# Optimization experiments

Measured on AMD Instinct MI355X. Metric: run time of the kernel, lower is better.

## Reference

```python
import jax, jax.numpy as jnp
import numpy as np

N_NODES = 50000


def gcn_conv(x, W, b, src, dst):
    # PyG GCNConv: lin (no bias) -> add self-loops -> symmetric deg norm ->
    # scatter-add messages to target nodes -> add bias.
    n = x.shape[0]
    xw = x @ W  # [N, H]
    loops = jnp.arange(n, dtype=src.dtype)
    s = jnp.concatenate([src, loops])
    d = jnp.concatenate([dst, loops])
    deg = jax.ops.segment_sum(jnp.ones(d.shape[0], dtype=x.dtype), d, num_segments=n)
    dinv = deg ** -0.5  # deg >= 1 due to self-loops
    norm = dinv[s] * dinv[d]  # [E+N]
    msg = xw[s] * norm[:, None]  # gather + scale, [E+N, H]
    out = jax.ops.segment_sum(msg, d, num_segments=n)  # scatter-add
    return out + b


def setup_inputs() -> dict:
    key = jax.random.key(0)
    ks = jax.random.split(key, 8)
    in_feats, hidden, out_feats, p = 64, 64, 32, 4
    x = jax.random.normal(ks[0], (N_NODES, in_feats), dtype=jnp.float32)
    edge_index = jax.random.randint(ks[1], (2, 800000), 0, N_NODES, dtype=jnp.int64)
    s1 = (1.0 / in_feats) ** 0.5
    s2 = (1.0 / hidden) ** 0.5
    W1 = jax.random.uniform(ks[2], (in_feats, hidden), jnp.float32, -s1, s1)
    b1 = jnp.zeros((hidden,), jnp.float32)
    W2 = jax.random.uniform(ks[3], (hidden, hidden), jnp.float32, -s2, s2)
    b2 = jnp.zeros((hidden,), jnp.float32)
    Wr = jax.random.uniform(ks[4], (hidden, out_feats * p), jnp.float32, -s2, s2)
    br = jax.random.uniform(ks[5], (out_feats * p,), jnp.float32, -s2, s2)
    return {"x": x, "edge_index": edge_index, "W1": W1, "b1": b1,
            "W2": W2, "b2": b2, "Wr": Wr, "br": br}


def reference(x, edge_index, W1, b1, W2, b2, Wr, br):
    src, dst = edge_index[0], edge_index[1]
    h = jax.nn.relu(gcn_conv(x, W1, b1, src, dst))
    h = jax.nn.relu(gcn_conv(h, W2, b2, src, dst))
    g = jnp.mean(h, axis=0, keepdims=True)  # [1, hidden]
    out = (g @ Wr + br).reshape(32, 4)  # (out_feats, p)
    return out
```

## Files before the change

### kernel.cpp

```cpp
#include <hip/hip_runtime.h>
#include <math.h>


#define CH 4096
#define MAXNB 1024

__global__ __launch_bounds__(256) void k_bucket_hist(const int* __restrict__ dst,
                                                     int* __restrict__ histmat,
                                                     int E, int NB) {
    __shared__ int ih[MAXNB];
    int t = threadIdx.x;
    for (int k = t; k < NB; k += 256) ih[k] = 0;
    __syncthreads();
    int base = blockIdx.x * CH;
    for (int i = 0; i < CH; i += 256) {
        int e = base + i + t;
        if (e < E) atomicAdd(&ih[dst[e] >> 6], 1);
    }
    __syncthreads();
    for (int k = t; k < NB; k += 256) histmat[(size_t)blockIdx.x * NB + k] = ih[k];
}

__global__ __launch_bounds__(256) void k_colscan(int* __restrict__ histmat,
                                                 int* __restrict__ tot,
                                                 int NB, int nch) {
    int k = blockIdx.x * 256 + threadIdx.x;
    if (k >= NB) return;
    int run = 0;
    int b = 0;
    for (; b + 8 <= nch; b += 8) {
        int v[8];
#pragma unroll
        for (int u = 0; u < 8; u++) v[u] = histmat[(size_t)(b + u) * NB + k];
#pragma unroll
        for (int u = 0; u < 8; u++) {
            int x = v[u];
            histmat[(size_t)(b + u) * NB + k] = run;
            run += x;
        }
    }
    for (; b < nch; b++) {
        int x = histmat[(size_t)b * NB + k];
        histmat[(size_t)b * NB + k] = run;
        run += x;
    }
    tot[k] = run;
}

__global__ __launch_bounds__(256) void k_scanb(const int* __restrict__ tot,
                                               int* __restrict__ bstart,
                                               int* __restrict__ offsets,
                                               int NB, int E, int n) {
    __shared__ int sc[256];
    __shared__ int carry;
    int t = threadIdx.x;
    if (t == 0) carry = 0;
    __syncthreads();
    int nchunk = (NB + 255) / 256;
    for (int c = 0; c < nchunk; c++) {
        int idx = c * 256 + t;
        int v = (idx < NB) ? tot[idx] : 0;
        sc[t] = v;
        __syncthreads();
        for (int off = 1; off < 256; off <<= 1) {
            int x = (t >= off) ? sc[t - off] : 0;
            __syncthreads();
            sc[t] += x;
            __syncthreads();
        }
        if (idx < NB) bstart[idx] = sc[t] - v + carry;
        __syncthreads();
        if (t == 0) carry += sc[255];
        __syncthreads();
    }
    if (t == 0) { bstart[NB] = E; offsets[n] = E; }
}

__global__ __launch_bounds__(256) void k_bucket_scatter(const int* __restrict__ src,
                                                        const int* __restrict__ dst,
                                                        const int* __restrict__ histmat,
                                                        const int* __restrict__ bstart,
                                                        int* __restrict__ staged,
                                                        int E, int NB) {
    __shared__ int cur[MAXNB];
    int t = threadIdx.x;
    for (int k = t; k < NB; k += 256)
        cur[k] = bstart[k] + histmat[(size_t)blockIdx.x * NB + k];
    __syncthreads();
    int base = blockIdx.x * CH;
    for (int i = 0; i < CH; i += 256) {
        int e = base + i + t;
        if (e < E) {
            int d = dst[e];
            int pos = atomicAdd(&cur[d >> 6], 1);
            staged[pos] = (src[e] << 6) | (d & 63);
        }
    }
}

__global__ __launch_bounds__(256) void k_local_sort(const int* __restrict__ staged,
                                                    const int* __restrict__ bstart,
                                                    int* __restrict__ csr_src,
                                                    int* __restrict__ offsets,
                                                    float* __restrict__ dinv, int n) {
    __shared__ int cnt[64];
    __shared__ int pos[64];
    __shared__ int cur[64];
    int t = threadIdx.x;
    if (t < 64) cnt[t] = 0;
    __syncthreads();
    int k = blockIdx.x;
    int beg = bstart[k], end = bstart[k + 1];
    for (int e = beg + t; e < end; e += 256) atomicAdd(&cnt[staged[e] & 63], 1);
    __syncthreads();
    if (t == 0) {
        int run = 0;
        for (int i = 0; i < 64; i++) { pos[i] = run; run += cnt[i]; }
    }
    __syncthreads();
    if (t < 64) {
        cur[t] = pos[t];
        int node = k * 64 + t;
        if (node < n) {
            offsets[node] = beg + pos[t];
            dinv[node] = 1.0f / sqrtf((float)(cnt[t] + 1));
        }
    }
    __syncthreads();
    for (int e = beg + t; e < end; e += 256) {
        int pk = staged[e];
        int p = atomicAdd(&cur[pk & 63], 1);
        csr_src[beg + p] = pk >> 6;
    }
}

__global__ __launch_bounds__(256) void k_gemm_scale(const float* __restrict__ X,
                                                    const float* __restrict__ W,
                                                    const float* __restrict__ dinv,
                                                    float* __restrict__ Y, int n) {
    __shared__ float Ws[64 * 64];
    __shared__ float xs[16][64];
    int t = threadIdx.x, w = t >> 6, f = t & 63;
    const float4* W4 = (const float4*)W;
    float4* Ws4 = (float4*)Ws;
#pragma unroll
    for (int j = 0; j < 4; j++) Ws4[t + 256 * j] = W4[t + 256 * j];
    int r0 = blockIdx.x * 16;
#pragma unroll
    for (int i = 0; i < 4; i++) {
        int r = r0 + w * 4 + i;
        xs[w * 4 + i][f] = (r < n) ? X[(size_t)r * 64 + f] : 0.f;
    }
    __syncthreads();
    float acc[4] = {0.f, 0.f, 0.f, 0.f};
#pragma unroll 8
    for (int k = 0; k < 64; k++) {
        float wv = Ws[k * 64 + f];
#pragma unroll
        for (int i = 0; i < 4; i++) acc[i] += xs[w * 4 + i][k] * wv;
    }
#pragma unroll
    for (int i = 0; i < 4; i++) {
        int r = r0 + w * 4 + i;
        if (r < n) Y[(size_t)r * 64 + f] = dinv[r] * acc[i];
    }
}

template <bool POOL>
__global__ __launch_bounds__(256) void k_aggregate(const float* __restrict__ Y,
                                                   const float* __restrict__ dinv,
                                                   const float* __restrict__ bias,
                                                   const int* __restrict__ offsets,
                                                   const int* __restrict__ csr_src,
                                                   float* __restrict__ H,
                                                   float* __restrict__ pbuf, int n) {
    __shared__ float4 sm4[4][16];
    const float4* Y4 = (const float4*)Y;
    int t = threadIdx.x, w = t >> 6, l = t & 63;
    int q = l >> 4, c = l & 15;
    int node = blockIdx.x * 4 + w;
    bool valid = node < n;
    float4 hval = make_float4(0.f, 0.f, 0.f, 0.f);
    if (valid) {
        float4 acc = make_float4(0.f, 0.f, 0.f, 0.f);
        if (q == 0) acc = Y4[(size_t)node * 16 + c];
        int beg = offsets[node], end = offsets[node + 1];
        for (int j = beg + q; j < end; j += 16) {
#pragma unroll
            for (int u = 0; u < 4; u++) {
                int jj = j + 4 * u;
                bool ok = jj < end;
                float4 v = make_float4(0.f, 0.f, 0.f, 0.f);
                if (ok) {
                    int s = csr_src[jj];
                    v = Y4[(size_t)s * 16 + c];
                }
                acc.x += v.x; acc.y += v.y; acc.z += v.z; acc.w += v.w;
            }
        }
#pragma unroll
        for (int m = 16; m <= 32; m <<= 1) {
            acc.x += __shfl_xor(acc.x, m);
            acc.y += __shfl_xor(acc.y, m);
            acc.z += __shfl_xor(acc.z, m);
            acc.w += __shfl_xor(acc.w, m);
        }
        float dv = dinv[node];
        float4 b4 = ((const float4*)bias)[c];
        hval.x = fmaxf(dv * acc.x + b4.x, 0.f);
        hval.y = fmaxf(dv * acc.y + b4.y, 0.f);
        hval.z = fmaxf(dv * acc.z + b4.z, 0.f);
        hval.w = fmaxf(dv * acc.w + b4.w, 0.f);
        if (!POOL && q == 0) ((float4*)H)[(size_t)node * 16 + c] = hval;
    }
    if (POOL) {
        if (q == 0) sm4[w][c] = valid ? hval : make_float4(0.f, 0.f, 0.f, 0.f);
        __syncthreads();
        if (t < 16) {
            float4 a = sm4[0][t], b = sm4[1][t], d = sm4[2][t], e = sm4[3][t];
            float4 s;
            s.x = (a.x + b.x) + (d.x + e.x);
            s.y = (a.y + b.y) + (d.y + e.y);
            s.z = (a.z + b.z) + (d.z + e.z);
            s.w = (a.w + b.w) + (d.w + e.w);
            ((float4*)pbuf)[(size_t)blockIdx.x * 16 + t] = s;
        }
    }
}

__global__ void k_mean_final(const float* __restrict__ pbuf, float* __restrict__ g,
                             int nrows) {
    __shared__ float part[256];
    int t = threadIdx.x, w = t >> 6, f = t & 63;
    float local = 0.f;
    for (int r = blockIdx.x * 4 + w; r < nrows; r += gridDim.x * 4)
        local += pbuf[(size_t)r * 64 + f];
    part[t] = local;
    __syncthreads();
    if (w == 0) {
        float tot = part[f] + part[64 + f] + part[128 + f] + part[192 + f];
        atomicAdd(&g[f], tot);
    }
}

__global__ void k_readout(const float* __restrict__ g, const float* __restrict__ Wr,
                          const float* __restrict__ br, float* __restrict__ out,
                          float invn) {
    __shared__ float gl[64];
    int t = threadIdx.x;
    if (t < 64) gl[t] = g[t] * invn;
    __syncthreads();
    float acc = br[t];
#pragma unroll
    for (int k = 0; k < 64; k++) acc += gl[k] * Wr[k * 128 + t];
    out[t] = acc;
}

extern "C" void kernel_launch(void* const* d_in, const int* in_sizes, int n_in,
                              void* d_out, int out_size, void* d_ws, size_t ws_size,
                              hipStream_t stream) {
    const float* x  = (const float*)d_in[0];
    const int*   ei = (const int*)d_in[1];
    const float* W1 = (const float*)d_in[2];
    const float* b1 = (const float*)d_in[3];
    const float* W2 = (const float*)d_in[4];
    const float* b2 = (const float*)d_in[5];
    const float* Wr = (const float*)d_in[6];
    const float* br = (const float*)d_in[7];
    float* out = (float*)d_out;

    int n = in_sizes[0] / 64;
    int E = in_sizes[1] / 2;
    const int* src = ei;
    const int* dst = ei + E;

    int NB  = (n + 63) / 64;
    int nch = (E + CH - 1) / CH;

    char* p = (char*)d_ws;
    float* y = (float*)p;      p += (size_t)n * 64 * sizeof(float);
    float* h = (float*)p;      p += (size_t)n * 64 * sizeof(float);
    float* dinv = (float*)p;   p += (size_t)n * sizeof(float);
    float* g = (float*)p;      p += 64 * sizeof(float);
    int* staged = (int*)p;     p += (size_t)E * sizeof(int);
    int* csr_src = (int*)p;    p += (size_t)E * sizeof(int);
    int* offsets = (int*)p;    p += (size_t)(n + 1) * sizeof(int);
    int* histmat = (int*)p;    p += (size_t)nch * NB * sizeof(int);
    int* tot = (int*)p;        p += (size_t)NB * sizeof(int);
    int* bstart = (int*)p;     p += (size_t)(NB + 1) * sizeof(int);

    int gb = (n + 3) / 4;

    hipMemsetAsync(g, 0, 64 * sizeof(float), stream);
    k_bucket_hist<<<nch, 256, 0, stream>>>(dst, histmat, E, NB);
    k_colscan<<<(NB + 255) / 256, 256, 0, stream>>>(histmat, tot, NB, nch);
    k_scanb<<<1, 256, 0, stream>>>(tot, bstart, offsets, NB, E, n);
    k_bucket_scatter<<<nch, 256, 0, stream>>>(src, dst, histmat, bstart, staged, E, NB);
    k_local_sort<<<NB, 256, 0, stream>>>(staged, bstart, csr_src, offsets, dinv, n);

    k_gemm_scale<<<(n + 15) / 16, 256, 0, stream>>>(x, W1, dinv, y, n);
    k_aggregate<false><<<gb, 256, 0, stream>>>(y, dinv, b1, offsets, csr_src, h, nullptr, n);
    k_gemm_scale<<<(n + 15) / 16, 256, 0, stream>>>(h, W2, dinv, y, n);
    float* pbuf = h;
    k_aggregate<true><<<gb, 256, 0, stream>>>(y, dinv, b2, offsets, csr_src, nullptr, pbuf, n);

    k_mean_final<<<64, 256, 0, stream>>>(pbuf, g, gb);
    k_readout<<<1, 128, 0, stream>>>(g, Wr, br, out, 1.0f / (float)n);
}
```

Before: 231.6 us.

## Fuse layer-2 GEMM into layer-1 aggregation and prefetch CSR indices via shuffles

The second layer's dense transform (h @ W2 scaled by dinv) now runs inside the first aggregation kernel. W2 is staged in shared memory and each wave's aggregated row is broadcast by shuffles, so the separate GEMM kernel and the write and re-read of the intermediate h buffer go away. The aggregation loop also loads up to 64 neighbor indices per node once per wave and distributes them with __shfl, instead of each lane re-reading csr_src. The cost is 16KB of shared memory per block plus a W2 load per block, which may reduce occupancy and adds per-block setup.

```diff
diff --git a/kernel.cpp b/kernel.cpp
--- a/kernel.cpp
+++ b/kernel.cpp
@@ -166,35 +166,46 @@
     }
 }
 
-template <bool POOL>
+template <bool FUSE, bool POOL>
 __global__ __launch_bounds__(256) void k_aggregate(const float* __restrict__ Y,
                                                    const float* __restrict__ dinv,
                                                    const float* __restrict__ bias,
                                                    const int* __restrict__ offsets,
                                                    const int* __restrict__ csr_src,
-                                                   float* __restrict__ H,
+                                                   const float* __restrict__ Wf,
+                                                   float* __restrict__ Yout,
                                                    float* __restrict__ pbuf, int n) {
+    __shared__ float Wfs[64 * 64];
     __shared__ float4 sm4[4][16];
-    const float4* Y4 = (const float4*)Y;
     int t = threadIdx.x, w = t >> 6, l = t & 63;
     int q = l >> 4, c = l & 15;
+    if (FUSE) {
+        const float4* W4 = (const float4*)Wf;
+        float4* Ws4 = (float4*)Wfs;
+#pragma unroll
+        for (int j = 0; j < 4; j++) Ws4[t + 256 * j] = W4[t + 256 * j];
+        __syncthreads();
+    }
+    const float4* Y4 = (const float4*)Y;
     int node = blockIdx.x * 4 + w;
     bool valid = node < n;
     float4 hval = make_float4(0.f, 0.f, 0.f, 0.f);
+    float dv = 0.f;
     if (valid) {
-        float4 acc = make_float4(0.f, 0.f, 0.f, 0.f);
-        if (q == 0) acc = Y4[(size_t)node * 16 + c];
         int beg = offsets[node], end = offsets[node + 1];
-        for (int j = beg + q; j < end; j += 16) {
+        int deg = end - beg;
+        int sidx = (l < deg) ? csr_src[beg + l] : 0;
+        float4 acc = (q == 0) ? Y4[(size_t)node * 16 + c]
+                              : make_float4(0.f, 0.f, 0.f, 0.f);
+        for (int e0 = 0; e0 < deg; e0 += 16) {
 #pragma unroll
             for (int u = 0; u < 4; u++) {
-                int jj = j + 4 * u;
-                bool ok = jj < end;
+                int e = e0 + u * 4 + q;
+                int s_sh = __shfl(sidx, e & 63);
+                bool ok = e < deg;
+                int s = (e < 64) ? s_sh : (ok ? csr_src[beg + e] : 0);
                 float4 v = make_float4(0.f, 0.f, 0.f, 0.f);
-                if (ok) {
-                    int s = csr_src[jj];
-                    v = Y4[(size_t)s * 16 + c];
-                }
+                if (ok) v = Y4[(size_t)s * 16 + c];
                 acc.x += v.x; acc.y += v.y; acc.z += v.z; acc.w += v.w;
             }
         }
@@ -205,13 +216,29 @@
             acc.z += __shfl_xor(acc.z, m);
             acc.w += __shfl_xor(acc.w, m);
         }
-        float dv = dinv[node];
+        dv = dinv[node];
         float4 b4 = ((const float4*)bias)[c];
         hval.x = fmaxf(dv * acc.x + b4.x, 0.f);
         hval.y = fmaxf(dv * acc.y + b4.y, 0.f);
         hval.z = fmaxf(dv * acc.z + b4.z, 0.f);
         hval.w = fmaxf(dv * acc.w + b4.w, 0.f);
-        if (!POOL && q == 0) ((float4*)H)[(size_t)node * 16 + c] = hval;
+    }
+    if (FUSE) {
+        if (valid) {
+            float acc2 = 0.f;
+#pragma unroll
+            for (int m = 0; m < 16; m++) {
+                float rx = __shfl(hval.x, m);
+                float ry = __shfl(hval.y, m);
+                float rz = __shfl(hval.z, m);
+                float rw = __shfl(hval.w, m);
+                acc2 += rx * Wfs[(4 * m + 0) * 64 + l] + ry * Wfs[(4 * m + 1) * 64 + l]
+                      + rz * Wfs[(4 * m + 2) * 64 + l] + rw * Wfs[(4 * m + 3) * 64 + l];
+            }
+            Yout[(size_t)node * 64 + l] = dv * acc2;
+        }
+    } else if (!POOL) {
+        if (valid && q == 0) ((float4*)Yout)[(size_t)node * 16 + c] = hval;
     }
     if (POOL) {
         if (q == 0) sm4[w][c] = valid ? hval : make_float4(0.f, 0.f, 0.f, 0.f);
@@ -278,8 +305,8 @@
     int nch = (E + CH - 1) / CH;
 
     char* p = (char*)d_ws;
-    float* y = (float*)p;      p += (size_t)n * 64 * sizeof(float);
-    float* h = (float*)p;      p += (size_t)n * 64 * sizeof(float);
+    float* y1 = (float*)p;     p += (size_t)n * 64 * sizeof(float);
+    float* y2 = (float*)p;     p += (size_t)n * 64 * sizeof(float);
     float* dinv = (float*)p;   p += (size_t)n * sizeof(float);
     float* g = (float*)p;      p += 64 * sizeof(float);
     int* staged = (int*)p;     p += (size_t)E * sizeof(int);
@@ -298,11 +325,12 @@
     k_bucket_scatter<<<nch, 256, 0, stream>>>(src, dst, histmat, bstart, staged, E, NB);
     k_local_sort<<<NB, 256, 0, stream>>>(staged, bstart, csr_src, offsets, dinv, n);
 
-    k_gemm_scale<<<(n + 15) / 16, 256, 0, stream>>>(x, W1, dinv, y, n);
-    k_aggregate<false><<<gb, 256, 0, stream>>>(y, dinv, b1, offsets, csr_src, h, nullptr, n);
-    k_gemm_scale<<<(n + 15) / 16, 256, 0, stream>>>(h, W2, dinv, y, n);
-    float* pbuf = h;
-    k_aggregate<true><<<gb, 256, 0, stream>>>(y, dinv, b2, offsets, csr_src, nullptr, pbuf, n);
+    k_gemm_scale<<<(n + 15) / 16, 256, 0, stream>>>(x, W1, dinv, y1, n);
+    k_aggregate<true, false><<<gb, 256, 0, stream>>>(y1, dinv, b1, offsets, csr_src,
+                                                     W2, y2, nullptr, n);
+    float* pbuf = y1;
+    k_aggregate<false, true><<<gb, 256, 0, stream>>>(y2, dinv, b2, offsets, csr_src,
+                                                     nullptr, nullptr, pbuf, n);
 
     k_mean_final<<<64, 256, 0, stream>>>(pbuf, g, gb);
     k_readout<<<1, 128, 0, stream>>>(g, Wr, br, out, 1.0f / (float)n);
```

New measurement: 234.7 us. No clear change (+1.4%).

## Split features into quarter planes and store CSR indices as 16-bit

Applied to the files above, without the earlier changes.

The GEMM output is stored as four feature-quarter planes of 16 floats per node, and aggregation runs one pass per plane (4x grid). This keeps each gathered working set (50000x64B) small enough to stay cache resident and improves locality of random neighbor gathers. CSR source indices shrink to unsigned short to halve index traffic, which only holds while node ids stay below 65536. The pooling reduction and mean kernel are adapted to the new per-pass layout.

```diff
diff --git a/kernel.cpp b/kernel.cpp
--- a/kernel.cpp
+++ b/kernel.cpp
@@ -100,7 +100,7 @@
 
 __global__ __launch_bounds__(256) void k_local_sort(const int* __restrict__ staged,
                                                     const int* __restrict__ bstart,
-                                                    int* __restrict__ csr_src,
+                                                    unsigned short* __restrict__ csr,
                                                     int* __restrict__ offsets,
                                                     float* __restrict__ dinv, int n) {
     __shared__ int cnt[64];
@@ -130,10 +130,11 @@
     for (int e = beg + t; e < end; e += 256) {
         int pk = staged[e];
         int p = atomicAdd(&cur[pk & 63], 1);
-        csr_src[beg + p] = pk >> 6;
-    }
-}
-
+        csr[beg + p] = (unsigned short)(pk >> 6);
+    }
+}
+
+template <bool QIN>
 __global__ __launch_bounds__(256) void k_gemm_scale(const float* __restrict__ X,
                                                     const float* __restrict__ W,
                                                     const float* __restrict__ dinv,
@@ -149,7 +150,11 @@
 #pragma unroll
     for (int i = 0; i < 4; i++) {
         int r = r0 + w * 4 + i;
-        xs[w * 4 + i][f] = (r < n) ? X[(size_t)r * 64 + f] : 0.f;
+        float v = 0.f;
+        if (r < n)
+            v = QIN ? X[((size_t)(f >> 4) * n + r) * 16 + (f & 15)]
+                    : X[(size_t)r * 64 + f];
+        xs[w * 4 + i][f] = v;
     }
     __syncthreads();
     float acc[4] = {0.f, 0.f, 0.f, 0.f};
@@ -162,68 +167,79 @@
 #pragma unroll
     for (int i = 0; i < 4; i++) {
         int r = r0 + w * 4 + i;
-        if (r < n) Y[(size_t)r * 64 + f] = dinv[r] * acc[i];
-    }
+        if (r < n) Y[((size_t)(f >> 4) * n + r) * 16 + (f & 15)] = dinv[r] * acc[i];
+    }
+}
+
+__device__ __forceinline__ float4 xor4(float4 a, int m) {
+    a.x += __shfl_xor(a.x, m);
+    a.y += __shfl_xor(a.y, m);
+    a.z += __shfl_xor(a.z, m);
+    a.w += __shfl_xor(a.w, m);
+    return a;
 }
 
 template <bool POOL>
-__global__ __launch_bounds__(256) void k_aggregate(const float* __restrict__ Y,
-                                                   const float* __restrict__ dinv,
-                                                   const float* __restrict__ bias,
-                                                   const int* __restrict__ offsets,
-                                                   const int* __restrict__ csr_src,
-                                                   float* __restrict__ H,
-                                                   float* __restrict__ pbuf, int n) {
-    __shared__ float4 sm4[4][16];
-    const float4* Y4 = (const float4*)Y;
+__global__ __launch_bounds__(256) void k_aggregate_q(const float* __restrict__ Y,
+                                                     const float* __restrict__ dinv,
+                                                     const float* __restrict__ bias,
+                                                     const int* __restrict__ offsets,
+                                                     const unsigned short* __restrict__ csr,
+                                                     float* __restrict__ Yout,
+                                                     float* __restrict__ pbuf,
+                                                     int n, int nblk) {
+    __shared__ float4 sm4[4][4];
     int t = threadIdx.x, w = t >> 6, l = t & 63;
-    int q = l >> 4, c = l & 15;
-    int node = blockIdx.x * 4 + w;
+    int i = l >> 4, j = (l >> 2) & 3, c = l & 3;
+    int pass = blockIdx.x / nblk, blk = blockIdx.x - pass * nblk;
+    int node = blk * 16 + w * 4 + i;
+    const float4* Y4 = (const float4*)Y + (size_t)pass * n * 4;
     bool valid = node < n;
-    float4 hval = make_float4(0.f, 0.f, 0.f, 0.f);
+    float4 acc = make_float4(0.f, 0.f, 0.f, 0.f);
+    float dv = 0.f;
     if (valid) {
-        float4 acc = make_float4(0.f, 0.f, 0.f, 0.f);
-        if (q == 0) acc = Y4[(size_t)node * 16 + c];
-        int beg = offsets[node], end = offsets[node + 1];
-        for (int j = beg + q; j < end; j += 16) {
+        int beg = offsets[node];
+        int deg = offsets[node + 1] - beg;
+        dv = dinv[node];
+        if (j == 0) acc = Y4[(size_t)node * 4 + c];
+        for (int e0 = 0; e0 < deg; e0 += 16) {
 #pragma unroll
             for (int u = 0; u < 4; u++) {
-                int jj = j + 4 * u;
-                bool ok = jj < end;
-                float4 v = make_float4(0.f, 0.f, 0.f, 0.f);
-                if (ok) {
-                    int s = csr_src[jj];
-                    v = Y4[(size_t)s * 16 + c];
+                int e = e0 + u * 4 + j;
+                if (e < deg) {
+                    int s = csr[beg + e];
+                    float4 v = Y4[(size_t)s * 4 + c];
+                    acc.x += v.x; acc.y += v.y; acc.z += v.z; acc.w += v.w;
                 }
-                acc.x += v.x; acc.y += v.y; acc.z += v.z; acc.w += v.w;
             }
         }
-#pragma unroll
-        for (int m = 16; m <= 32; m <<= 1) {
-            acc.x += __shfl_xor(acc.x, m);
-            acc.y += __shfl_xor(acc.y, m);
-            acc.z += __shfl_xor(acc.z, m);
-            acc.w += __shfl_xor(acc.w, m);
-        }
-        float dv = dinv[node];
-        float4 b4 = ((const float4*)bias)[c];
-        hval.x = fmaxf(dv * acc.x + b4.x, 0.f);
-        hval.y = fmaxf(dv * acc.y + b4.y, 0.f);
-        hval.z = fmaxf(dv * acc.z + b4.z, 0.f);
-        hval.w = fmaxf(dv * acc.w + b4.w, 0.f);
-        if (!POOL && q == 0) ((float4*)H)[(size_t)node * 16 + c] = hval;
-    }
-    if (POOL) {
-        if (q == 0) sm4[w][c] = valid ? hval : make_float4(0.f, 0.f, 0.f, 0.f);
+    }
+    acc = xor4(acc, 4);
+    acc = xor4(acc, 8);
+    float4 b4 = ((const float4*)bias)[pass * 4 + c];
+    float4 h = make_float4(0.f, 0.f, 0.f, 0.f);
+    if (valid) {
+        h.x = fmaxf(dv * acc.x + b4.x, 0.f);
+        h.y = fmaxf(dv * acc.y + b4.y, 0.f);
+        h.z = fmaxf(dv * acc.z + b4.z, 0.f);
+        h.w = fmaxf(dv * acc.w + b4.w, 0.f);
+    }
+    if (!POOL) {
+        if (valid && j == 0)
+            ((float4*)Yout + (size_t)pass * n * 4)[(size_t)node * 4 + c] = h;
+    } else {
+        h = xor4(h, 16);
+        h = xor4(h, 32);
+        if (l < 4) sm4[w][c] = h;
         __syncthreads();
-        if (t < 16) {
+        if (t < 4) {
             float4 a = sm4[0][t], b = sm4[1][t], d = sm4[2][t], e = sm4[3][t];
             float4 s;
             s.x = (a.x + b.x) + (d.x + e.x);
             s.y = (a.y + b.y) + (d.y + e.y);
             s.z = (a.z + b.z) + (d.z + e.z);
             s.w = (a.w + b.w) + (d.w + e.w);
-            ((float4*)pbuf)[(size_t)blockIdx.x * 16 + t] = s;
+            ((float4*)pbuf)[((size_t)blk * 4 + pass) * 4 + t] = s;
         }
     }
 }
@@ -274,36 +290,37 @@
     const int* src = ei;
     const int* dst = ei + E;
 
-    int NB  = (n + 63) / 64;
-    int nch = (E + CH - 1) / CH;
+    int NB   = (n + 63) / 64;
+    int nch  = (E + CH - 1) / CH;
+    int nblk = (n + 15) / 16;
 
     char* p = (char*)d_ws;
-    float* y = (float*)p;      p += (size_t)n * 64 * sizeof(float);
-    float* h = (float*)p;      p += (size_t)n * 64 * sizeof(float);
+    float* y1 = (float*)p;     p += (size_t)n * 64 * sizeof(float);
+    float* y2 = (float*)p;     p += (size_t)n * 64 * sizeof(float);
     float* dinv = (float*)p;   p += (size_t)n * sizeof(float);
     float* g = (float*)p;      p += 64 * sizeof(float);
     int* staged = (int*)p;     p += (size_t)E * sizeof(int);
-    int* csr_src = (int*)p;    p += (size_t)E * sizeof(int);
     int* offsets = (int*)p;    p += (size_t)(n + 1) * sizeof(int);
     int* histmat = (int*)p;    p += (size_t)nch * NB * sizeof(int);
     int* tot = (int*)p;        p += (size_t)NB * sizeof(int);
     int* bstart = (int*)p;     p += (size_t)(NB + 1) * sizeof(int);
-
-    int gb = (n + 3) / 4;
+    unsigned short* csr = (unsigned short*)p; p += (size_t)E * sizeof(unsigned short);
 
     hipMemsetAsync(g, 0, 64 * sizeof(float), stream);
     k_bucket_hist<<<nch, 256, 0, stream>>>(dst, histmat, E, NB);
     k_colscan<<<(NB + 255) / 256, 256, 0, stream>>>(histmat, tot, NB, nch);
     k_scanb<<<1, 256, 0, stream>>>(tot, bstart, offsets, NB, E, n);
     k_bucket_scatter<<<nch, 256, 0, stream>>>(src, dst, histmat, bstart, staged, E, NB);
-    k_local_sort<<<NB, 256, 0, stream>>>(staged, bstart, csr_src, offsets, dinv, n);
-
-    k_gemm_scale<<<(n + 15) / 16, 256, 0, stream>>>(x, W1, dinv, y, n);
-    k_aggregate<false><<<gb, 256, 0, stream>>>(y, dinv, b1, offsets, csr_src, h, nullptr, n);
-    k_gemm_scale<<<(n + 15) / 16, 256, 0, stream>>>(h, W2, dinv, y, n);
-    float* pbuf = h;
-    k_aggregate<true><<<gb, 256, 0, stream>>>(y, dinv, b2, offsets, csr_src, nullptr, pbuf, n);
-
-    k_mean_final<<<64, 256, 0, stream>>>(pbuf, g, gb);
+    k_local_sort<<<NB, 256, 0, stream>>>(staged, bstart, csr, offsets, dinv, n);
+
+    k_gemm_scale<false><<<(n + 15) / 16, 256, 0, stream>>>(x, W1, dinv, y1, n);
+    k_aggregate_q<false><<<4 * nblk, 256, 0, stream>>>(y1, dinv, b1, offsets, csr,
+                                                       y2, nullptr, n, nblk);
+    k_gemm_scale<true><<<(n + 15) / 16, 256, 0, stream>>>(y2, W2, dinv, y1, n);
+    float* pbuf = y2;
+    k_aggregate_q<true><<<4 * nblk, 256, 0, stream>>>(y1, dinv, b2, offsets, csr,
+                                                      nullptr, pbuf, n, nblk);
+
+    k_mean_final<<<64, 256, 0, stream>>>(pbuf, g, nblk);
     k_readout<<<1, 128, 0, stream>>>(g, Wr, br, out, 1.0f / (float)n);
 }
```

After: 233.7 us. No clear change (+0.9%).

## Fuse CSR build into one cooperative kernel and store 16-bit source indices

Applied to the files above, without the earlier changes.

Merges histogram, column scan, bucket scan, bucket scatter and local sort into a single cooperative kernel over 256 blocks, with grid-wide syncs between phases. This removes several launches and the memset. It also stores CSR source indices as unsigned short to halve index traffic in the aggregation gathers. The 16-bit index only holds for node counts below 65536, and the per-block chunks are now larger with fewer blocks running the scatter phases.

```diff
diff --git a/kernel.cpp b/kernel.cpp
--- a/kernel.cpp
+++ b/kernel.cpp
@@ -1,136 +1,119 @@
 #include <hip/hip_runtime.h>
+#include <hip/hip_cooperative_groups.h>
 #include <math.h>
 
-
-#define CH 4096
+namespace cg = cooperative_groups;
+
+
 #define MAXNB 1024
-
-__global__ __launch_bounds__(256) void k_bucket_hist(const int* __restrict__ dst,
-                                                     int* __restrict__ histmat,
-                                                     int E, int NB) {
-    __shared__ int ih[MAXNB];
-    int t = threadIdx.x;
-    for (int k = t; k < NB; k += 256) ih[k] = 0;
-    __syncthreads();
-    int base = blockIdx.x * CH;
-    for (int i = 0; i < CH; i += 256) {
-        int e = base + i + t;
-        if (e < E) atomicAdd(&ih[dst[e] >> 6], 1);
-    }
-    __syncthreads();
-    for (int k = t; k < NB; k += 256) histmat[(size_t)blockIdx.x * NB + k] = ih[k];
-}
-
-__global__ __launch_bounds__(256) void k_colscan(int* __restrict__ histmat,
-                                                 int* __restrict__ tot,
-                                                 int NB, int nch) {
-    int k = blockIdx.x * 256 + threadIdx.x;
-    if (k >= NB) return;
-    int run = 0;
-    int b = 0;
-    for (; b + 8 <= nch; b += 8) {
-        int v[8];
-#pragma unroll
-        for (int u = 0; u < 8; u++) v[u] = histmat[(size_t)(b + u) * NB + k];
-#pragma unroll
-        for (int u = 0; u < 8; u++) {
-            int x = v[u];
-            histmat[(size_t)(b + u) * NB + k] = run;
-            run += x;
-        }
-    }
-    for (; b < nch; b++) {
-        int x = histmat[(size_t)b * NB + k];
-        histmat[(size_t)b * NB + k] = run;
-        run += x;
-    }
-    tot[k] = run;
-}
-
-__global__ __launch_bounds__(256) void k_scanb(const int* __restrict__ tot,
+#define GB 256
+
+__global__ __launch_bounds__(256) void k_build(const int* __restrict__ src,
+                                               const int* __restrict__ dst,
+                                               int* __restrict__ histmat,
+                                               int* __restrict__ tot,
                                                int* __restrict__ bstart,
+                                               int* __restrict__ staged,
+                                               unsigned short* __restrict__ csr,
                                                int* __restrict__ offsets,
-                                               int NB, int E, int n) {
+                                               float* __restrict__ dinv,
+                                               float* __restrict__ g,
+                                               int E, int n, int NB, int CH2) {
+    cg::grid_group grid = cg::this_grid();
+    __shared__ int sm[MAXNB];
     __shared__ int sc[256];
     __shared__ int carry;
-    int t = threadIdx.x;
-    if (t == 0) carry = 0;
-    __syncthreads();
-    int nchunk = (NB + 255) / 256;
-    for (int c = 0; c < nchunk; c++) {
-        int idx = c * 256 + t;
-        int v = (idx < NB) ? tot[idx] : 0;
-        sc[t] = v;
-        __syncthreads();
-        for (int off = 1; off < 256; off <<= 1) {
-            int x = (t >= off) ? sc[t - off] : 0;
+    __shared__ int cnt[64], pref[64], cur[64];
+    int t = threadIdx.x, b = blockIdx.x;
+    if (b == 0 && t < 64) g[t] = 0.f;
+
+    for (int k = t; k < NB; k += 256) sm[k] = 0;
+    __syncthreads();
+    int base = b * CH2;
+    int lim = min(E, base + CH2);
+    for (int e = base + t; e < lim; e += 256) atomicAdd(&sm[dst[e] >> 6], 1);
+    __syncthreads();
+    for (int k = t; k < NB; k += 256) histmat[(size_t)b * NB + k] = sm[k];
+    grid.sync();
+
+    int kk = b * 256 + t;
+    if (kk < NB) {
+        int run = 0;
+        for (int c = 0; c < GB; c += 8) {
+            int v[8];
+#pragma unroll
+            for (int u = 0; u < 8; u++) v[u] = histmat[(size_t)(c + u) * NB + kk];
+#pragma unroll
+            for (int u = 0; u < 8; u++) {
+                int x = v[u];
+                histmat[(size_t)(c + u) * NB + kk] = run;
+                run += x;
+            }
+        }
+        tot[kk] = run;
+    }
+    grid.sync();
+
+    if (b == 0) {
+        if (t == 0) carry = 0;
+        __syncthreads();
+        int nchunk = (NB + 255) / 256;
+        for (int c = 0; c < nchunk; c++) {
+            int idx = c * 256 + t;
+            int v = (idx < NB) ? tot[idx] : 0;
+            sc[t] = v;
             __syncthreads();
-            sc[t] += x;
+            for (int off = 1; off < 256; off <<= 1) {
+                int x = (t >= off) ? sc[t - off] : 0;
+                __syncthreads();
+                sc[t] += x;
+                __syncthreads();
+            }
+            if (idx < NB) bstart[idx] = sc[t] - v + carry;
             __syncthreads();
-        }
-        if (idx < NB) bstart[idx] = sc[t] - v + carry;
-        __syncthreads();
-        if (t == 0) carry += sc[255];
-        __syncthreads();
-    }
-    if (t == 0) { bstart[NB] = E; offsets[n] = E; }
-}
-
-__global__ __launch_bounds__(256) void k_bucket_scatter(const int* __restrict__ src,
-                                                        const int* __restrict__ dst,
-                                                        const int* __restrict__ histmat,
-                                                        const int* __restrict__ bstart,
-                                                        int* __restrict__ staged,
-                                                        int E, int NB) {
-    __shared__ int cur[MAXNB];
-    int t = threadIdx.x;
+            if (t == 0) carry += sc[255];
+            __syncthreads();
+        }
+        if (t == 0) { bstart[NB] = E; offsets[n] = E; }
+    }
+    grid.sync();
+
     for (int k = t; k < NB; k += 256)
-        cur[k] = bstart[k] + histmat[(size_t)blockIdx.x * NB + k];
-    __syncthreads();
-    int base = blockIdx.x * CH;
-    for (int i = 0; i < CH; i += 256) {
-        int e = base + i + t;
-        if (e < E) {
-            int d = dst[e];
-            int pos = atomicAdd(&cur[d >> 6], 1);
-            staged[pos] = (src[e] << 6) | (d & 63);
-        }
-    }
-}
-
-__global__ __launch_bounds__(256) void k_local_sort(const int* __restrict__ staged,
-                                                    const int* __restrict__ bstart,
-                                                    int* __restrict__ csr_src,
-                                                    int* __restrict__ offsets,
-                                                    float* __restrict__ dinv, int n) {
-    __shared__ int cnt[64];
-    __shared__ int pos[64];
-    __shared__ int cur[64];
-    int t = threadIdx.x;
-    if (t < 64) cnt[t] = 0;
-    __syncthreads();
-    int k = blockIdx.x;
-    int beg = bstart[k], end = bstart[k + 1];
-    for (int e = beg + t; e < end; e += 256) atomicAdd(&cnt[staged[e] & 63], 1);
-    __syncthreads();
-    if (t == 0) {
-        int run = 0;
-        for (int i = 0; i < 64; i++) { pos[i] = run; run += cnt[i]; }
-    }
-    __syncthreads();
-    if (t < 64) {
-        cur[t] = pos[t];
-        int node = k * 64 + t;
-        if (node < n) {
-            offsets[node] = beg + pos[t];
-            dinv[node] = 1.0f / sqrtf((float)(cnt[t] + 1));
-        }
-    }
-    __syncthreads();
-    for (int e = beg + t; e < end; e += 256) {
-        int pk = staged[e];
-        int p = atomicAdd(&cur[pk & 63], 1);
-        csr_src[beg + p] = pk >> 6;
+        sm[k] = bstart[k] + histmat[(size_t)b * NB + k];
+    __syncthreads();
+    for (int e = base + t; e < lim; e += 256) {
+        int d = dst[e];
+        int pos = atomicAdd(&sm[d >> 6], 1);
+        staged[pos] = (src[e] << 6) | (d & 63);
+    }
+    grid.sync();
+
+    for (int k = b; k < NB; k += gridDim.x) {
+        if (t < 64) cnt[t] = 0;
+        __syncthreads();
+        int beg = bstart[k], end = bstart[k + 1];
+        for (int e = beg + t; e < end; e += 256) atomicAdd(&cnt[staged[e] & 63], 1);
+        __syncthreads();
+        if (t == 0) {
+            int run = 0;
+            for (int i = 0; i < 64; i++) { pref[i] = run; run += cnt[i]; }
+        }
+        __syncthreads();
+        if (t < 64) {
+            cur[t] = pref[t];
+            int node = k * 64 + t;
+            if (node < n) {
+                offsets[node] = beg + pref[t];
+                dinv[node] = 1.0f / sqrtf((float)(cnt[t] + 1));
+            }
+        }
+        __syncthreads();
+        for (int e = beg + t; e < end; e += 256) {
+            int pk = staged[e];
+            int p = atomicAdd(&cur[pk & 63], 1);
+            csr[beg + p] = (unsigned short)(pk >> 6);
+        }
+        __syncthreads();
     }
 }
 
@@ -171,7 +154,7 @@
                                                    const float* __restrict__ dinv,
                                                    const float* __restrict__ bias,
                                                    const int* __restrict__ offsets,
-                                                   const int* __restrict__ csr_src,
+                                                   const unsigned short* __restrict__ csr,
                                                    float* __restrict__ H,
                                                    float* __restrict__ pbuf, int n) {
     __shared__ float4 sm4[4][16];
@@ -192,7 +175,7 @@
                 bool ok = jj < end;
                 float4 v = make_float4(0.f, 0.f, 0.f, 0.f);
                 if (ok) {
-                    int s = csr_src[jj];
+                    int s = csr[jj];
                     v = Y4[(size_t)s * 16 + c];
                 }
                 acc.x += v.x; acc.y += v.y; acc.z += v.z; acc.w += v.w;
@@ -275,34 +258,30 @@
     const int* dst = ei + E;
 
     int NB  = (n + 63) / 64;
-    int nch = (E + CH - 1) / CH;
+    int CH2 = (E + GB - 1) / GB;
 
     char* p = (char*)d_ws;
-    float* y = (float*)p;      p += (size_t)n * 64 * sizeof(float);
-    float* h = (float*)p;      p += (size_t)n * 64 * sizeof(float);
+    float* y1 = (float*)p;     p += (size_t)n * 64 * sizeof(float);
+    float* y2 = (float*)p;     p += (size_t)n * 64 * sizeof(float);
     float* dinv = (float*)p;   p += (size_t)n * sizeof(float);
     float* g = (float*)p;      p += 64 * sizeof(float);
     int* staged = (int*)p;     p += (size_t)E * sizeof(int);
-    int* csr_src = (int*)p;    p += (size_t)E * sizeof(int);
     int* offsets = (int*)p;    p += (size_t)(n + 1) * sizeof(int);
-    int* histmat = (int*)p;    p += (size_t)nch * NB * sizeof(int);
+    int* histmat = (int*)p;    p += (size_t)GB * NB * sizeof(int);
     int* tot = (int*)p;        p += (size_t)NB * sizeof(int);
     int* bstart = (int*)p;     p += (size_t)(NB + 1) * sizeof(int);
+    unsigned short* csr = (unsigned short*)p; p += (size_t)E * sizeof(unsigned short);
+
+    void* bargs[] = {&src, &dst, &histmat, &tot, &bstart, &staged, &csr,
+                     &offsets, &dinv, &g, &E, &n, &NB, &CH2};
+    hipLaunchCooperativeKernel((void*)k_build, dim3(GB), dim3(256), bargs, 0, stream);
 
     int gb = (n + 3) / 4;
-
-    hipMemsetAsync(g, 0, 64 * sizeof(float), stream);
-    k_bucket_hist<<<nch, 256, 0, stream>>>(dst, histmat, E, NB);
-    k_colscan<<<(NB + 255) / 256, 256, 0, stream>>>(histmat, tot, NB, nch);
-    k_scanb<<<1, 256, 0, stream>>>(tot, bstart, offsets, NB, E, n);
-    k_bucket_scatter<<<nch, 256, 0, stream>>>(src, dst, histmat, bstart, staged, E, NB);
-    k_local_sort<<<NB, 256, 0, stream>>>(staged, bstart, csr_src, offsets, dinv, n);
-
-    k_gemm_scale<<<(n + 15) / 16, 256, 0, stream>>>(x, W1, dinv, y, n);
-    k_aggregate<false><<<gb, 256, 0, stream>>>(y, dinv, b1, offsets, csr_src, h, nullptr, n);
-    k_gemm_scale<<<(n + 15) / 16, 256, 0, stream>>>(h, W2, dinv, y, n);
-    float* pbuf = h;
-    k_aggregate<true><<<gb, 256, 0, stream>>>(y, dinv, b2, offsets, csr_src, nullptr, pbuf, n);
+    k_gemm_scale<<<(n + 15) / 16, 256, 0, stream>>>(x, W1, dinv, y1, n);
+    k_aggregate<false><<<gb, 256, 0, stream>>>(y1, dinv, b1, offsets, csr, y2, nullptr, n);
+    k_gemm_scale<<<(n + 15) / 16, 256, 0, stream>>>(y2, W2, dinv, y1, n);
+    float* pbuf = y2;
+    k_aggregate<true><<<gb, 256, 0, stream>>>(y1, dinv, b2, offsets, csr, nullptr, pbuf, n);
 
     k_mean_final<<<64, 256, 0, stream>>>(pbuf, g, gb);
     k_readout<<<1, 128, 0, stream>>>(g, Wr, br, out, 1.0f / (float)n);
```

After: 367.1 us. 1.58x slower.
